# Kernel tuning notes

Measured on AMD Instinct MI355X. Metric: run time of the kernel, lower is better.

The kernel has to match this reference:

```python
import jax, jax.numpy as jnp
import numpy as np

N = 100000   # nodes
E = 1600000  # edges
S = 4        # state_dimension
H = 64       # hidden_channels


def _gcn_conv(x, row, col, W, b):
    """PyG GCNConv: h = x @ W; add self-loops; symmetric deg^-1/2 norm; scatter-add; + bias."""
    n = x.shape[0]
    h = x @ W  # [N, out]
    loop = jnp.arange(n, dtype=row.dtype)
    r = jnp.concatenate([row, loop])  # sources (with self-loops)
    c = jnp.concatenate([col, loop])  # targets (with self-loops)
    deg = jax.ops.segment_sum(jnp.ones(r.shape[0], h.dtype), c, num_segments=n)
    dinv = jnp.where(deg > 0, jax.lax.rsqrt(deg), 0.0)
    norm = dinv[r] * dinv[c]                      # [E+N]
    msg = h[r] * norm[:, None]                    # gather + scale, [E+N, out]
    out = jax.ops.segment_sum(msg, c, num_segments=n)  # scatter-add
    return out + b


def setup_inputs() -> dict:
    key = jax.random.key(0)
    k1, k2, k3, k4 = jax.random.split(key, 4)
    x = jax.random.normal(k1, (N, S), dtype=jnp.float32)
    edge_index = jax.random.randint(k2, (2, E), 0, N, dtype=jnp.int32)
    # Glorot-ish init for the two GCNConv linear layers (+ zero bias, PyG default)
    W1 = jax.random.normal(k3, (S, H), dtype=jnp.float32) * (1.0 / np.sqrt(S))
    b1 = jnp.zeros((H,), jnp.float32)
    W2 = jax.random.normal(k4, (H, S), dtype=jnp.float32) * (1.0 / np.sqrt(H))
    b2 = jnp.zeros((S,), jnp.float32)
    return {"x": x, "edge_index": edge_index, "W1": W1, "b1": b1, "W2": W2, "b2": b2}


def reference(x, edge_index, W1, b1, W2, b2):
    row, col = edge_index[0], edge_index[1]
    h = _gcn_conv(x, row, col, W1, b1)
    h = jax.nn.relu(h)
    out = _gcn_conv(h, row, col, W2, b2)
    return out
```

## Files before the change

kernel.cpp:

```cpp
#include <hip/hip_runtime.h>


#define BSHIFT 7
#define BNODES 128
#define KMAX   1024
#define CAP    3072
#define EPB    8192
#define FTH    512
#define CURPAD 16

__global__ void k_zero(int* __restrict__ p, int n) {
    int i = blockIdx.x * blockDim.x + threadIdx.x;
    if (i < n) p[i] = 0;
}

__global__ void __launch_bounds__(FTH) k_fill(
        const int* __restrict__ row, const int* __restrict__ col,
        int e, int K, int* __restrict__ cursor, unsigned* __restrict__ ere) {
    __shared__ int h[KMAX];
    __shared__ int loff[KMAX];
    __shared__ int gbase[KMAX];
    __shared__ int lcur[KMAX];
    __shared__ int cs[128];
    __shared__ unsigned staged[EPB];

    int t = threadIdx.x;
    for (int k = t; k < KMAX; k += FTH) { h[k] = 0; lcur[k] = 0; }
    __syncthreads();

    int lo = blockIdx.x * EPB;
    int cbuf[16];
#pragma unroll
    for (int k = 0; k < 16; ++k) {
        int i = lo + t + k * FTH;
        cbuf[k] = (i < e) ? col[i] : -1;
    }
#pragma unroll
    for (int k = 0; k < 16; ++k)
        if (cbuf[k] >= 0) atomicAdd(&h[cbuf[k] >> BSHIFT], 1);
    __syncthreads();

    if (t < 128) {
        int s = 0;
#pragma unroll
        for (int j = 0; j < 8; ++j) s += h[t * 8 + j];
        cs[t] = s;
    }
    __syncthreads();
    for (int off = 1; off < 128; off <<= 1) {
        int v = (t < 128 && t >= off) ? cs[t - off] : 0;
        __syncthreads();
        if (t < 128) cs[t] += v;
        __syncthreads();
    }
    if (t < 128) {
        int run = t ? cs[t - 1] : 0;
#pragma unroll
        for (int j = 0; j < 8; ++j) { loff[t * 8 + j] = run; run += h[t * 8 + j]; }
    }
    for (int k = t; k < K; k += FTH)
        if (h[k]) gbase[k] = atomicAdd(&cursor[k * CURPAD], h[k]);
    __syncthreads();

#pragma unroll
    for (int k = 0; k < 16; ++k) {
        int c = cbuf[k];
        if (c < 0) continue;
        int i = lo + t + k * FTH;
        int b = c >> BSHIFT;
        int pos = loff[b] + atomicAdd(&lcur[b], 1);
        staged[pos] = ((unsigned)row[i] << BSHIFT) | (unsigned)(c & (BNODES - 1));
    }
    __syncthreads();

    int wid = t >> 6, lane = t & 63, nw = FTH >> 6;
    for (int k = wid; k < K; k += nw) {
        int len = h[k];
        if (!len) continue;
        int gb = gbase[k], lb = loff[k];
        size_t dst = (size_t)k * CAP + gb;
        for (int j = lane; j < len; j += 64)
            if (gb + j < CAP) ere[dst + j] = staged[lb + j];
    }
}

__global__ void __launch_bounds__(256) k_sort(
        const int* __restrict__ cursor, unsigned* __restrict__ ere,
        int* __restrict__ rstart, const float4* __restrict__ x,
        float* __restrict__ dinv, float4* __restrict__ y, int n) {
    __shared__ unsigned recs[CAP];
    __shared__ unsigned sorted[CAP];
    __shared__ int hist[BNODES];
    __shared__ int sc[BNODES];
    __shared__ int lcur[BNODES];
    int b = blockIdx.x, t = threadIdx.x, nlo = b << BSHIFT;
    if (t < BNODES) hist[t] = 0;
    __syncthreads();
    size_t c0 = (size_t)b * CAP;
    int m = min(cursor[b * CURPAD], CAP);
    int n4 = m >> 2;
    const uint4* e4 = (const uint4*)(ere + c0);
    for (int g = t; g < n4; g += 256) {
        uint4 w = e4[g];
        ((uint4*)recs)[g] = w;
        atomicAdd(&hist[w.x & (BNODES - 1)], 1);
        atomicAdd(&hist[w.y & (BNODES - 1)], 1);
        atomicAdd(&hist[w.z & (BNODES - 1)], 1);
        atomicAdd(&hist[w.w & (BNODES - 1)], 1);
    }
    for (int i = (n4 << 2) + t; i < m; i += 256) {
        unsigned w = ere[c0 + i];
        recs[i] = w;
        atomicAdd(&hist[w & (BNODES - 1)], 1);
    }
    __syncthreads();
    if (t < BNODES) sc[t] = hist[t];
    __syncthreads();
    for (int off = 1; off < BNODES; off <<= 1) {
        int v = (t < BNODES && t >= off) ? sc[t - off] : 0;
        __syncthreads();
        if (t < BNODES) sc[t] += v;
        __syncthreads();
    }
    if (t < BNODES) {
        int st = sc[t] - hist[t];
        lcur[t] = st;
        rstart[b * BNODES + t] = st;
        int node = nlo + t;
        if (node < n) {
            float di = rsqrtf((float)hist[t] + 1.0f);
            dinv[node] = di;
            float4 xv = x[node];
            y[node] = make_float4(xv.x * di, xv.y * di, xv.z * di, xv.w * di);
        }
    }
    __syncthreads();
    for (int i = t; i < m; i += 256) {
        unsigned w = recs[i];
        int pos = atomicAdd(&lcur[w & (BNODES - 1)], 1);
        sorted[pos] = w >> BSHIFT;
    }
    __syncthreads();
    uint4* o4 = (uint4*)(ere + c0);
    for (int g = t; g < n4; g += 256) o4[g] = ((uint4*)sorted)[g];
    for (int i = (n4 << 2) + t; i < m; i += 256) ere[c0 + i] = sorted[i];
}

__global__ void __launch_bounds__(256) k_mid1(
        const unsigned* __restrict__ ere, const int* __restrict__ cursor,
        const int* __restrict__ rstart, const float* __restrict__ dinv,
        const float4* __restrict__ x, const float4* __restrict__ y,
        const float* __restrict__ W1, const float* __restrict__ b1,
        const float* __restrict__ W2, const float* __restrict__ b2,
        float4* __restrict__ z, float4* __restrict__ out, int n) {
    __shared__ unsigned recs[CAP];
    __shared__ float4 sums[BNODES];
    int b = blockIdx.x, t = threadIdx.x, nlo = b << BSHIFT;
    size_t c0 = (size_t)b * CAP;
    int m = min(cursor[b * CURPAD], CAP);
    int n4 = m >> 2;
    const uint4* e4 = (const uint4*)(ere + c0);
    for (int g = t; g < n4; g += 256) ((uint4*)recs)[g] = e4[g];
    for (int i = (n4 << 2) + t; i < m; i += 256) recs[i] = ere[c0 + i];
    __syncthreads();
    int tt = t >> 1, half = t & 1;
    int s = rstart[b * BNODES + tt];
    int epos = (tt < BNODES - 1) ? rstart[b * BNODES + tt + 1] : m;
    float vx = 0.f, vy = 0.f, vz = 0.f, vw = 0.f;
    int i = s + half;
    while (i + 6 < epos) {
        int r0 = recs[i], r1 = recs[i + 2], r2 = recs[i + 4], r3 = recs[i + 6];
        float4 a0 = y[r0], a1 = y[r1], a2 = y[r2], a3 = y[r3];
        vx += a0.x + a1.x + a2.x + a3.x;
        vy += a0.y + a1.y + a2.y + a3.y;
        vz += a0.z + a1.z + a2.z + a3.z;
        vw += a0.w + a1.w + a2.w + a3.w;
        i += 8;
    }
    for (; i < epos; i += 2) {
        float4 a = y[recs[i]];
        vx += a.x; vy += a.y; vz += a.z; vw += a.w;
    }
    vx += __shfl_xor(vx, 1);
    vy += __shfl_xor(vy, 1);
    vz += __shfl_xor(vz, 1);
    vw += __shfl_xor(vw, 1);
    if (half == 0) sums[tt] = make_float4(vx, vy, vz, vw);
    __syncthreads();
    int node = nlo + t;
    if (t < BNODES && node < n) {
        float di = dinv[node], sl = di * di;
        float4 sv = sums[t];
        float4 xv = x[node];
        float a0 = di * sv.x + xv.x * sl;
        float a1 = di * sv.y + xv.y * sl;
        float a2 = di * sv.z + xv.z * sl;
        float a3 = di * sv.w + xv.w * sl;
        float t0 = 0.f, t1 = 0.f, t2 = 0.f, t3 = 0.f;
#pragma unroll 8
        for (int j = 0; j < 64; ++j) {
            float h = b1[j] + a0 * W1[j] + a1 * W1[64 + j] + a2 * W1[128 + j] + a3 * W1[192 + j];
            h = fmaxf(h, 0.f);
            t0 += h * W2[j * 4 + 0];
            t1 += h * W2[j * 4 + 1];
            t2 += h * W2[j * 4 + 2];
            t3 += h * W2[j * 4 + 3];
        }
        z[node] = make_float4(t0 * di, t1 * di, t2 * di, t3 * di);
        out[node] = make_float4(b2[0] + t0 * sl, b2[1] + t1 * sl,
                                b2[2] + t2 * sl, b2[3] + t3 * sl);
    }
}

__global__ void __launch_bounds__(256) k_acc2(
        const unsigned* __restrict__ ere, const int* __restrict__ cursor,
        const int* __restrict__ rstart, const float* __restrict__ dinv,
        const float4* __restrict__ z, float4* __restrict__ out, int n) {
    __shared__ unsigned recs[CAP];
    int b = blockIdx.x, t = threadIdx.x, nlo = b << BSHIFT;
    size_t c0 = (size_t)b * CAP;
    int m = min(cursor[b * CURPAD], CAP);
    int n4 = m >> 2;
    const uint4* e4 = (const uint4*)(ere + c0);
    for (int g = t; g < n4; g += 256) ((uint4*)recs)[g] = e4[g];
    for (int i = (n4 << 2) + t; i < m; i += 256) recs[i] = ere[c0 + i];
    __syncthreads();
    int tt = t >> 1, half = t & 1;
    int s = rstart[b * BNODES + tt];
    int epos = (tt < BNODES - 1) ? rstart[b * BNODES + tt + 1] : m;
    float vx = 0.f, vy = 0.f, vz = 0.f, vw = 0.f;
    int i = s + half;
    while (i + 6 < epos) {
        int r0 = recs[i], r1 = recs[i + 2], r2 = recs[i + 4], r3 = recs[i + 6];
        float4 a0 = z[r0], a1 = z[r1], a2 = z[r2], a3 = z[r3];
        vx += a0.x + a1.x + a2.x + a3.x;
        vy += a0.y + a1.y + a2.y + a3.y;
        vz += a0.z + a1.z + a2.z + a3.z;
        vw += a0.w + a1.w + a2.w + a3.w;
        i += 8;
    }
    for (; i < epos; i += 2) {
        float4 a = z[recs[i]];
        vx += a.x; vy += a.y; vz += a.z; vw += a.w;
    }
    vx += __shfl_xor(vx, 1);
    vy += __shfl_xor(vy, 1);
    vz += __shfl_xor(vz, 1);
    vw += __shfl_xor(vw, 1);
    int node = nlo + tt;
    if (half == 0 && node < n) {
        float di = dinv[node];
        float4 o = out[node];
        out[node] = make_float4(o.x + di * vx, o.y + di * vy,
                                o.z + di * vz, o.w + di * vw);
    }
}

extern "C" void kernel_launch(void* const* d_in, const int* in_sizes, int n_in,
                              void* d_out, int out_size, void* d_ws, size_t ws_size,
                              hipStream_t stream) {
    const float* x  = (const float*)d_in[0];
    const int* edge = (const int*)d_in[1];
    const float* W1 = (const float*)d_in[2];
    const float* b1 = (const float*)d_in[3];
    const float* W2 = (const float*)d_in[4];
    const float* b2 = (const float*)d_in[5];
    float* out = (float*)d_out;

    const int n = in_sizes[0] / 4;
    const int e = in_sizes[1] / 2;
    const int* row = edge;
    const int* col = edge + e;
    const int K = (n + BNODES - 1) >> BSHIFT;

    char* ws = (char*)d_ws;
    float* y    = (float*)ws;  ws += (size_t)4 * n * 4;
    float* zmid = (float*)ws;  ws += (size_t)4 * n * 4;
    float* dinv = (float*)ws;  ws += (size_t)n * 4;
    unsigned* ere = (unsigned*)ws;  ws += (size_t)K * CAP * 4;
    int* cursor = (int*)ws;    ws += (size_t)K * CURPAD * 4;
    int* rstart = (int*)ws;    ws += (size_t)K * BNODES * 4;

    const int B = 256;
    const int gf = (e + EPB - 1) / EPB;
    const int nz = K * CURPAD;

    k_zero<<<(nz + B - 1) / B, B, 0, stream>>>(cursor, nz);
    k_fill<<<gf, FTH, 0, stream>>>(row, col, e, K, cursor, ere);
    k_sort<<<K, B, 0, stream>>>(cursor, ere, rstart, (const float4*)x,
                                dinv, (float4*)y, n);
    k_mid1<<<K, B, 0, stream>>>(ere, cursor, rstart, dinv, (const float4*)x,
                                (const float4*)y, W1, b1, W2, b2,
                                (float4*)zmid, (float4*)out, n);
    k_acc2<<<K, B, 0, stream>>>(ere, cursor, rstart, dinv,
                                (const float4*)zmid, (float4*)out, n);
}
```

Before: 143.9 us.

## Partition edges into 1024-node buckets and decouple sort from gather block size

The edge bucketing moves from 782 buckets of 128 target nodes to 98 coarse buckets of 1024 nodes. Each bucket is then counting-sorted by a 1024-thread block, and rstart now holds absolute offsets into the edge array. Both gather kernels use 512-thread blocks covering 256 nodes each and load their edge slice through those offsets. The goal is fewer global atomic cursors and more contiguous scatter writes in the partition step. The cost is heavy per-block shared memory in the sort (about 80KB), which limits occupancy, and a risk of silently dropping edges if a bucket exceeds its fixed capacity.

```diff
diff --git a/kernel.cpp b/kernel.cpp
--- a/kernel.cpp
+++ b/kernel.cpp
@@ -1,171 +1,160 @@
 #include <hip/hip_runtime.h>
 
 
-#define BSHIFT 7
-#define BNODES 128
-#define KMAX   1024
-#define CAP    3072
-#define EPB    8192
-#define FTH    512
+#define CSHIFT 10
+#define CNODES 1024
+#define KC_MAX 128
+#define CAPC   18432
+#define EPB    4096
 #define CURPAD 16
+#define ANODES 256
+#define ACAP   4864
 
 __global__ void k_zero(int* __restrict__ p, int n) {
     int i = blockIdx.x * blockDim.x + threadIdx.x;
     if (i < n) p[i] = 0;
 }
 
-__global__ void __launch_bounds__(FTH) k_fill(
+__global__ void __launch_bounds__(256) k_part(
         const int* __restrict__ row, const int* __restrict__ col,
-        int e, int K, int* __restrict__ cursor, unsigned* __restrict__ ere) {
-    __shared__ int h[KMAX];
-    __shared__ int loff[KMAX];
-    __shared__ int gbase[KMAX];
-    __shared__ int lcur[KMAX];
-    __shared__ int cs[128];
+        int e, int Kc, int* __restrict__ cursor, unsigned* __restrict__ ere) {
+    __shared__ int h[KC_MAX];
+    __shared__ int loff[KC_MAX];
+    __shared__ int gbase[KC_MAX];
+    __shared__ int lcur[KC_MAX];
     __shared__ unsigned staged[EPB];
-
     int t = threadIdx.x;
-    for (int k = t; k < KMAX; k += FTH) { h[k] = 0; lcur[k] = 0; }
-    __syncthreads();
-
+    if (t < KC_MAX) h[t] = 0;
+    __syncthreads();
     int lo = blockIdx.x * EPB;
-    int cbuf[16];
+    int cbuf[16], rbuf[16];
 #pragma unroll
     for (int k = 0; k < 16; ++k) {
-        int i = lo + t + k * FTH;
-        cbuf[k] = (i < e) ? col[i] : -1;
+        int i = lo + t + k * 256;
+        if (i < e) { cbuf[k] = col[i]; rbuf[k] = row[i]; }
+        else { cbuf[k] = -1; rbuf[k] = 0; }
     }
 #pragma unroll
     for (int k = 0; k < 16; ++k)
-        if (cbuf[k] >= 0) atomicAdd(&h[cbuf[k] >> BSHIFT], 1);
-    __syncthreads();
-
-    if (t < 128) {
-        int s = 0;
-#pragma unroll
-        for (int j = 0; j < 8; ++j) s += h[t * 8 + j];
-        cs[t] = s;
-    }
-    __syncthreads();
-    for (int off = 1; off < 128; off <<= 1) {
-        int v = (t < 128 && t >= off) ? cs[t - off] : 0;
-        __syncthreads();
-        if (t < 128) cs[t] += v;
-        __syncthreads();
-    }
-    if (t < 128) {
-        int run = t ? cs[t - 1] : 0;
-#pragma unroll
-        for (int j = 0; j < 8; ++j) { loff[t * 8 + j] = run; run += h[t * 8 + j]; }
-    }
-    for (int k = t; k < K; k += FTH)
-        if (h[k]) gbase[k] = atomicAdd(&cursor[k * CURPAD], h[k]);
-    __syncthreads();
-
+        if (cbuf[k] >= 0) atomicAdd(&h[cbuf[k] >> CSHIFT], 1);
+    __syncthreads();
+    if (t < KC_MAX) loff[t] = h[t];
+    __syncthreads();
+    for (int off = 1; off < KC_MAX; off <<= 1) {
+        int v = (t < KC_MAX && t >= off) ? loff[t - off] : 0;
+        __syncthreads();
+        if (t < KC_MAX) loff[t] += v;
+        __syncthreads();
+    }
+    if (t < KC_MAX) {
+        int st = loff[t] - h[t];
+        loff[t] = st;
+        lcur[t] = st;
+        if (t < Kc && h[t]) gbase[t] = atomicAdd(&cursor[t * CURPAD], h[t]);
+    }
+    __syncthreads();
 #pragma unroll
     for (int k = 0; k < 16; ++k) {
         int c = cbuf[k];
         if (c < 0) continue;
-        int i = lo + t + k * FTH;
-        int b = c >> BSHIFT;
-        int pos = loff[b] + atomicAdd(&lcur[b], 1);
-        staged[pos] = ((unsigned)row[i] << BSHIFT) | (unsigned)(c & (BNODES - 1));
-    }
-    __syncthreads();
-
-    int wid = t >> 6, lane = t & 63, nw = FTH >> 6;
-    for (int k = wid; k < K; k += nw) {
+        int pos = atomicAdd(&lcur[c >> CSHIFT], 1);
+        staged[pos] = ((unsigned)rbuf[k] << CSHIFT) | (unsigned)(c & (CNODES - 1));
+    }
+    __syncthreads();
+    int wid = t >> 6, lane = t & 63;
+    for (int k = wid; k < Kc; k += 4) {
         int len = h[k];
         if (!len) continue;
         int gb = gbase[k], lb = loff[k];
-        size_t dst = (size_t)k * CAP + gb;
+        size_t dst = (size_t)k * CAPC + gb;
         for (int j = lane; j < len; j += 64)
-            if (gb + j < CAP) ere[dst + j] = staged[lb + j];
-    }
-}
-
-__global__ void __launch_bounds__(256) k_sort(
+            if (gb + j < CAPC) ere[dst + j] = staged[lb + j];
+    }
+}
+
+__global__ void __launch_bounds__(1024) k_sortN(
         const int* __restrict__ cursor, unsigned* __restrict__ ere,
         int* __restrict__ rstart, const float4* __restrict__ x,
         float* __restrict__ dinv, float4* __restrict__ y, int n) {
-    __shared__ unsigned recs[CAP];
-    __shared__ unsigned sorted[CAP];
-    __shared__ int hist[BNODES];
-    __shared__ int sc[BNODES];
-    __shared__ int lcur[BNODES];
-    int b = blockIdx.x, t = threadIdx.x, nlo = b << BSHIFT;
-    if (t < BNODES) hist[t] = 0;
-    __syncthreads();
-    size_t c0 = (size_t)b * CAP;
-    int m = min(cursor[b * CURPAD], CAP);
+    __shared__ int hist[CNODES];
+    __shared__ int lcur[CNODES];
+    __shared__ unsigned sorted[CAPC];
+    int b = blockIdx.x, t = threadIdx.x, nlo = b << CSHIFT;
+    hist[t] = 0;
+    __syncthreads();
+    size_t c0 = (size_t)b * CAPC;
+    int m = min(cursor[b * CURPAD], CAPC);
     int n4 = m >> 2;
     const uint4* e4 = (const uint4*)(ere + c0);
-    for (int g = t; g < n4; g += 256) {
+    for (int g = t; g < n4; g += 1024) {
         uint4 w = e4[g];
-        ((uint4*)recs)[g] = w;
-        atomicAdd(&hist[w.x & (BNODES - 1)], 1);
-        atomicAdd(&hist[w.y & (BNODES - 1)], 1);
-        atomicAdd(&hist[w.z & (BNODES - 1)], 1);
-        atomicAdd(&hist[w.w & (BNODES - 1)], 1);
-    }
-    for (int i = (n4 << 2) + t; i < m; i += 256) {
+        atomicAdd(&hist[w.x & (CNODES - 1)], 1);
+        atomicAdd(&hist[w.y & (CNODES - 1)], 1);
+        atomicAdd(&hist[w.z & (CNODES - 1)], 1);
+        atomicAdd(&hist[w.w & (CNODES - 1)], 1);
+    }
+    for (int i = (n4 << 2) + t; i < m; i += 1024)
+        atomicAdd(&hist[ere[c0 + i] & (CNODES - 1)], 1);
+    __syncthreads();
+    int hv = hist[t];
+    lcur[t] = hv;
+    __syncthreads();
+    for (int off = 1; off < CNODES; off <<= 1) {
+        int v = (t >= off) ? lcur[t - off] : 0;
+        __syncthreads();
+        lcur[t] += v;
+        __syncthreads();
+    }
+    int st = lcur[t] - hv;
+    lcur[t] = st;
+    rstart[(b << CSHIFT) + t] = (int)c0 + st;
+    int node = nlo + t;
+    if (node < n) {
+        float di = rsqrtf((float)hv + 1.0f);
+        dinv[node] = di;
+        float4 xv = x[node];
+        y[node] = make_float4(xv.x * di, xv.y * di, xv.z * di, xv.w * di);
+    }
+    __syncthreads();
+    for (int g = t; g < n4; g += 1024) {
+        uint4 w = e4[g];
+        int p0 = atomicAdd(&lcur[w.x & (CNODES - 1)], 1); sorted[p0] = w.x >> CSHIFT;
+        int p1 = atomicAdd(&lcur[w.y & (CNODES - 1)], 1); sorted[p1] = w.y >> CSHIFT;
+        int p2 = atomicAdd(&lcur[w.z & (CNODES - 1)], 1); sorted[p2] = w.z >> CSHIFT;
+        int p3 = atomicAdd(&lcur[w.w & (CNODES - 1)], 1); sorted[p3] = w.w >> CSHIFT;
+    }
+    for (int i = (n4 << 2) + t; i < m; i += 1024) {
         unsigned w = ere[c0 + i];
-        recs[i] = w;
-        atomicAdd(&hist[w & (BNODES - 1)], 1);
-    }
-    __syncthreads();
-    if (t < BNODES) sc[t] = hist[t];
-    __syncthreads();
-    for (int off = 1; off < BNODES; off <<= 1) {
-        int v = (t < BNODES && t >= off) ? sc[t - off] : 0;
-        __syncthreads();
-        if (t < BNODES) sc[t] += v;
-        __syncthreads();
-    }
-    if (t < BNODES) {
-        int st = sc[t] - hist[t];
-        lcur[t] = st;
-        rstart[b * BNODES + t] = st;
-        int node = nlo + t;
-        if (node < n) {
-            float di = rsqrtf((float)hist[t] + 1.0f);
-            dinv[node] = di;
-            float4 xv = x[node];
-            y[node] = make_float4(xv.x * di, xv.y * di, xv.z * di, xv.w * di);
-        }
-    }
-    __syncthreads();
-    for (int i = t; i < m; i += 256) {
-        unsigned w = recs[i];
-        int pos = atomicAdd(&lcur[w & (BNODES - 1)], 1);
-        sorted[pos] = w >> BSHIFT;
+        int p = atomicAdd(&lcur[w & (CNODES - 1)], 1);
+        sorted[p] = w >> CSHIFT;
     }
     __syncthreads();
     uint4* o4 = (uint4*)(ere + c0);
-    for (int g = t; g < n4; g += 256) o4[g] = ((uint4*)sorted)[g];
-    for (int i = (n4 << 2) + t; i < m; i += 256) ere[c0 + i] = sorted[i];
-}
-
-__global__ void __launch_bounds__(256) k_mid1(
-        const unsigned* __restrict__ ere, const int* __restrict__ cursor,
-        const int* __restrict__ rstart, const float* __restrict__ dinv,
+    for (int g = t; g < n4; g += 1024) o4[g] = ((uint4*)sorted)[g];
+    for (int i = (n4 << 2) + t; i < m; i += 1024) ere[c0 + i] = sorted[i];
+}
+
+__global__ void __launch_bounds__(512) k_mid(
+        const unsigned* __restrict__ ere, const int* __restrict__ rstart,
+        const int* __restrict__ cursor, const float* __restrict__ dinv,
         const float4* __restrict__ x, const float4* __restrict__ y,
         const float* __restrict__ W1, const float* __restrict__ b1,
         const float* __restrict__ W2, const float* __restrict__ b2,
         float4* __restrict__ z, float4* __restrict__ out, int n) {
-    __shared__ unsigned recs[CAP];
-    __shared__ float4 sums[BNODES];
-    int b = blockIdx.x, t = threadIdx.x, nlo = b << BSHIFT;
-    size_t c0 = (size_t)b * CAP;
-    int m = min(cursor[b * CURPAD], CAP);
-    int n4 = m >> 2;
-    const uint4* e4 = (const uint4*)(ere + c0);
-    for (int g = t; g < n4; g += 256) ((uint4*)recs)[g] = e4[g];
-    for (int i = (n4 << 2) + t; i < m; i += 256) recs[i] = ere[c0 + i];
+    __shared__ unsigned recs[ACAP];
+    __shared__ float4 sums[ANODES];
+    int g = blockIdx.x, t = threadIdx.x;
+    int nlo = g * ANODES;
+    int b = nlo >> CSHIFT;
+    int s0 = rstart[nlo];
+    int e0 = ((g & 3) == 3) ? (int)((size_t)b * CAPC) + min(cursor[b * CURPAD], CAPC)
+                            : rstart[nlo + ANODES];
+    int len = min(e0 - s0, ACAP);
+    for (int i = t; i < len; i += 512) recs[i] = ere[s0 + i];
     __syncthreads();
     int tt = t >> 1, half = t & 1;
-    int s = rstart[b * BNODES + tt];
-    int epos = (tt < BNODES - 1) ? rstart[b * BNODES + tt + 1] : m;
+    int s = rstart[nlo + tt] - s0;
+    int epos = ((tt == ANODES - 1) ? len : min(rstart[nlo + tt + 1] - s0, len));
     float vx = 0.f, vy = 0.f, vz = 0.f, vw = 0.f;
     int i = s + half;
     while (i + 6 < epos) {
@@ -188,7 +177,7 @@
     if (half == 0) sums[tt] = make_float4(vx, vy, vz, vw);
     __syncthreads();
     int node = nlo + t;
-    if (t < BNODES && node < n) {
+    if (t < ANODES && node < n) {
         float di = dinv[node], sl = di * di;
         float4 sv = sums[t];
         float4 xv = x[node];
@@ -212,22 +201,23 @@
     }
 }
 
-__global__ void __launch_bounds__(256) k_acc2(
-        const unsigned* __restrict__ ere, const int* __restrict__ cursor,
-        const int* __restrict__ rstart, const float* __restrict__ dinv,
+__global__ void __launch_bounds__(512) k_acc2(
+        const unsigned* __restrict__ ere, const int* __restrict__ rstart,
+        const int* __restrict__ cursor, const float* __restrict__ dinv,
         const float4* __restrict__ z, float4* __restrict__ out, int n) {
-    __shared__ unsigned recs[CAP];
-    int b = blockIdx.x, t = threadIdx.x, nlo = b << BSHIFT;
-    size_t c0 = (size_t)b * CAP;
-    int m = min(cursor[b * CURPAD], CAP);
-    int n4 = m >> 2;
-    const uint4* e4 = (const uint4*)(ere + c0);
-    for (int g = t; g < n4; g += 256) ((uint4*)recs)[g] = e4[g];
-    for (int i = (n4 << 2) + t; i < m; i += 256) recs[i] = ere[c0 + i];
+    __shared__ unsigned recs[ACAP];
+    int g = blockIdx.x, t = threadIdx.x;
+    int nlo = g * ANODES;
+    int b = nlo >> CSHIFT;
+    int s0 = rstart[nlo];
+    int e0 = ((g & 3) == 3) ? (int)((size_t)b * CAPC) + min(cursor[b * CURPAD], CAPC)
+                            : rstart[nlo + ANODES];
+    int len = min(e0 - s0, ACAP);
+    for (int i = t; i < len; i += 512) recs[i] = ere[s0 + i];
     __syncthreads();
     int tt = t >> 1, half = t & 1;
-    int s = rstart[b * BNODES + tt];
-    int epos = (tt < BNODES - 1) ? rstart[b * BNODES + tt + 1] : m;
+    int s = rstart[nlo + tt] - s0;
+    int epos = ((tt == ANODES - 1) ? len : min(rstart[nlo + tt + 1] - s0, len));
     float vx = 0.f, vy = 0.f, vz = 0.f, vw = 0.f;
     int i = s + half;
     while (i + 6 < epos) {
@@ -271,27 +261,28 @@
     const int e = in_sizes[1] / 2;
     const int* row = edge;
     const int* col = edge + e;
-    const int K = (n + BNODES - 1) >> BSHIFT;
+    const int Kc = (n + CNODES - 1) >> CSHIFT;
 
     char* ws = (char*)d_ws;
     float* y    = (float*)ws;  ws += (size_t)4 * n * 4;
     float* zmid = (float*)ws;  ws += (size_t)4 * n * 4;
     float* dinv = (float*)ws;  ws += (size_t)n * 4;
-    unsigned* ere = (unsigned*)ws;  ws += (size_t)K * CAP * 4;
-    int* cursor = (int*)ws;    ws += (size_t)K * CURPAD * 4;
-    int* rstart = (int*)ws;    ws += (size_t)K * BNODES * 4;
+    unsigned* ere = (unsigned*)ws;  ws += (size_t)Kc * CAPC * 4;
+    int* cursor = (int*)ws;    ws += (size_t)Kc * CURPAD * 4;
+    int* rstart = (int*)ws;    ws += (size_t)Kc * CNODES * 4;
 
     const int B = 256;
-    const int gf = (e + EPB - 1) / EPB;
-    const int nz = K * CURPAD;
+    const int gp = (e + EPB - 1) / EPB;
+    const int ga = (n + ANODES - 1) / ANODES;
+    const int nz = Kc * CURPAD;
 
     k_zero<<<(nz + B - 1) / B, B, 0, stream>>>(cursor, nz);
-    k_fill<<<gf, FTH, 0, stream>>>(row, col, e, K, cursor, ere);
-    k_sort<<<K, B, 0, stream>>>(cursor, ere, rstart, (const float4*)x,
-                                dinv, (float4*)y, n);
-    k_mid1<<<K, B, 0, stream>>>(ere, cursor, rstart, dinv, (const float4*)x,
-                                (const float4*)y, W1, b1, W2, b2,
-                                (float4*)zmid, (float4*)out, n);
-    k_acc2<<<K, B, 0, stream>>>(ere, cursor, rstart, dinv,
-                                (const float4*)zmid, (float4*)out, n);
-}
+    k_part<<<gp, B, 0, stream>>>(row, col, e, Kc, cursor, ere);
+    k_sortN<<<Kc, 1024, 0, stream>>>(cursor, ere, rstart, (const float4*)x,
+                                     dinv, (float4*)y, n);
+    k_mid<<<ga, 512, 0, stream>>>(ere, rstart, cursor, dinv, (const float4*)x,
+                                  (const float4*)y, W1, b1, W2, b2,
+                                  (float4*)zmid, (float4*)out, n);
+    k_acc2<<<ga, 512, 0, stream>>>(ere, rstart, cursor, dinv,
+                                   (const float4*)zmid, (float4*)out, n);
+}
```

Result: faster. 127.7 us (-11.2%).
